# Optimization experiments

Hardware: AMD Instinct MI355X
Metric: run time of the kernel (lower is better)

## Reference

```python
import jax, jax.numpy as jnp
import numpy as np
import math

FACTOR = 100.0
WN_THRESH = 0.99

# extra MANO palm-closing faces from the original module
FACES_NEW = np.array([[92, 38, 234], [234, 38, 239], [38, 122, 239], [239, 122, 279],
                      [122, 118, 279], [279, 118, 215], [118, 117, 215], [215, 117, 214],
                      [117, 119, 214], [214, 119, 121], [119, 120, 121], [121, 120, 78],
                      [120, 108, 78], [78, 108, 79]], dtype=np.int64)


def solid_angles(points, triangles):
    # points: (B,Q,3); triangles: (B,F,3,3) -> (B,Q,F)
    ct = triangles[:, None] - points[:, :, None, None]        # (B,Q,F,3,3)
    norms = jnp.linalg.norm(ct, axis=-1)                      # (B,Q,F,3)
    cross = jnp.cross(ct[..., 1, :], ct[..., 2, :])           # (B,Q,F,3)
    numerator = jnp.sum(ct[..., 0, :] * cross, axis=-1)       # (B,Q,F)
    dot01 = jnp.sum(ct[..., 0, :] * ct[..., 1, :], axis=-1)
    dot12 = jnp.sum(ct[..., 1, :] * ct[..., 2, :], axis=-1)
    dot02 = jnp.sum(ct[..., 0, :] * ct[..., 2, :], axis=-1)
    denominator = (norms.prod(axis=-1) + dot01 * norms[..., 2]
                   + dot02 * norms[..., 1] + dot12 * norms[..., 0])
    return 2.0 * jnp.arctan2(numerator, denominator)


def winding_numbers(points, triangles):
    return solid_angles(points, triangles).sum(axis=-1) / (4.0 * math.pi)


def pairwise_dist(x, y, squared=False):
    # x: (B,N,3), y: (B,M,3) -> (B,N,M)
    xx = jnp.sum(x * x, axis=-1)
    yy = jnp.sum(y * y, axis=-1)
    zz = jnp.einsum('bnd,bmd->bnm', x, y)
    P = xx[:, :, None] + yy[:, None, :] - 2.0 * zz
    if not squared:
        P = jnp.sqrt(jnp.clip(P, 0.0))
    return P


def setup_inputs() -> dict:
    key = jax.random.key(0)
    k1, k2, k3 = jax.random.split(key, 3)
    B, Q, NF = 8, 778, 1538
    v1 = jax.random.normal(k1, (B, Q, 3), dtype=jnp.float32)
    v2 = jax.random.normal(k2, (B, Q, 3), dtype=jnp.float32)
    faces = jax.random.randint(k3, (NF, 3), 0, Q, dtype=jnp.int64)
    return {"v1": v1, "v2": v2, "faces": faces}


def reference(v1, v2, faces):
    r_faces = jnp.concatenate([faces, jnp.asarray(FACES_NEW)], axis=0)   # (F,3)
    l_faces = r_faces[:, jnp.array([0, 2, 1])]
    t1l = v1[:, l_faces, :]   # (B,F,3,3)
    t2l = v2[:, r_faces, :]
    interior_v1 = winding_numbers(v1, t2l) >= WN_THRESH   # (B,Q) bool
    interior_v2 = winding_numbers(v2, t1l) >= WN_THRESH

    d12 = pairwise_dist(v1, v2)       # (B,Q,Q)
    d21 = pairwise_dist(v2, v1)
    min12 = jnp.min(d12, axis=-1)     # (B,Q): dist from each v1 point to v2
    min21 = jnp.min(d21, axis=-1)

    pt1 = ((min12 * FACTOR) ** 2) * interior_v1.astype(v1.dtype)
    pt2 = ((min21 * FACTOR) ** 2) * interior_v2.astype(v2.dtype)
    bloss = pt1.sum(axis=-1) + pt2.sum(axis=-1)   # (B,)
    gate = jnp.any(interior_v1, axis=-1) & jnp.any(interior_v2, axis=-1)
    bloss = jnp.where(gate, bloss, 0.0)
    return bloss.mean()
```

## Files before the change

### kernel.cpp

```cpp
#include <hip/hip_runtime.h>
#include <math.h>

#define BQ 778
#define NF_IN 1538
#define NF_NEW 14
#define NT 1552
#define NB 8
#define BLOCK 1024
#define NWAVE 16
#define TRI_PER_WAVE 97

__constant__ int FACES_NEW_D[NF_NEW * 3] = {
    92, 38, 234, 234, 38, 239, 38, 122, 239, 239, 122, 279,
    122, 118, 279, 279, 118, 215, 118, 117, 215, 215, 117, 214,
    117, 119, 214, 214, 119, 121, 119, 120, 121, 121, 120, 78,
    120, 108, 78, 78, 108, 79};

__device__ __forceinline__ float fast_atan2f(float y, float x) {
  float ax = __builtin_fabsf(x), ay = __builtin_fabsf(y);
  float mx = fmaxf(ax, ay), mn = fminf(ax, ay);
  float r  = __builtin_amdgcn_rcpf(mx);
  float t  = mn * r;
  float e  = __builtin_fmaf(-t, mx, mn);
  t = __builtin_fmaf(e, r, t);
  float s = t * t;
  float u =                  0.00282363896258175373077393f;
  u = __builtin_fmaf(u, s, -0.0159569028764963150024414f);
  u = __builtin_fmaf(u, s,  0.0425049886107444763183594f);
  u = __builtin_fmaf(u, s, -0.0748900920152664184570312f);
  u = __builtin_fmaf(u, s,  0.106347933411598205566406f);
  u = __builtin_fmaf(u, s, -0.142027363181114196777344f);
  u = __builtin_fmaf(u, s,  0.199926957488059997558594f);
  u = __builtin_fmaf(u, s, -0.333331018686294555664062f);
  float a = __builtin_fmaf(u * s, t, t);
  a = (ay > ax) ? (1.57079632679489662f - a) : a;
  a = (x < 0.0f) ? (3.14159265358979323f - a) : a;
  return __builtin_copysignf(a, y);
}

__global__ __launch_bounds__(BLOCK) void wn_dist_kernel(
    const float* __restrict__ v1, const float* __restrict__ v2,
    const int* __restrict__ faces, float* __restrict__ sums,
    unsigned int* __restrict__ flags) {
  __shared__ float4 sv[BQ];
  __shared__ ushort4 sf4[NT];
  __shared__ float romega[NWAVE][64];
  __shared__ float rdmin[NWAVE][64];

  const int PG = 13;
  int bid = blockIdx.x;
  int cloud = bid / PG;
  int pg = bid % PG;
  int side = cloud >> 3;
  int b = cloud & 7;

  const float* pts = (side == 0) ? (v1 + b * BQ * 3) : (v2 + b * BQ * 3);
  const float* opp = (side == 0) ? (v2 + b * BQ * 3) : (v1 + b * BQ * 3);

  int tid = threadIdx.x;
  for (int i = tid; i < BQ; i += BLOCK) {
    sv[i] = make_float4(opp[i * 3 + 0], opp[i * 3 + 1], opp[i * 3 + 2], 0.0f);
  }
  for (int f = tid; f < NF_IN; f += BLOCK) {
    ushort4 u;
    u.x = (unsigned short)(faces[f * 3 + 0] << 4);
    u.y = (unsigned short)(faces[f * 3 + 1] << 4);
    u.z = (unsigned short)(faces[f * 3 + 2] << 4);
    u.w = 0;
    sf4[f] = u;
  }
  for (int f = tid; f < NF_NEW; f += BLOCK) {
    ushort4 u;
    u.x = (unsigned short)(FACES_NEW_D[f * 3 + 0] << 4);
    u.y = (unsigned short)(FACES_NEW_D[f * 3 + 1] << 4);
    u.z = (unsigned short)(FACES_NEW_D[f * 3 + 2] << 4);
    u.w = 0;
    sf4[NF_IN + f] = u;
  }
  __syncthreads();

  int wave = tid >> 6;
  int lane = tid & 63;
  int q = pg * 64 + lane;
  bool valid = (q < BQ);
  int qc = valid ? q : (BQ - 1);

  const float sgn = side ? -1.0f : 1.0f;
  float px = pts[qc * 3 + 0];
  float py = pts[qc * 3 + 1];
  float pz = pts[qc * 3 + 2];

  const char* svb = (const char*)sv;

  float omega = 0.0f;
  int tbase = wave * TRI_PER_WAVE;
  for (int k = 0; k < TRI_PER_WAVE; ++k) {
    ushort4 f = sf4[tbase + k];
    float4 va = *(const float4*)(svb + f.x);
    float4 vb = *(const float4*)(svb + f.y);
    float4 vc = *(const float4*)(svb + f.z);
    float ax = va.x - px, ay = va.y - py, az = va.z - pz;
    float bx = vb.x - px, by = vb.y - py, bz = vb.z - pz;
    float cx = vc.x - px, cy = vc.y - py, cz = vc.z - pz;
    float la = sqrtf(ax * ax + ay * ay + az * az);
    float lb = sqrtf(bx * bx + by * by + bz * bz);
    float lc = sqrtf(cx * cx + cy * cy + cz * cz);
    float crx = by * cz - bz * cy;
    float cry = bz * cx - bx * cz;
    float crz = bx * cy - by * cx;
    float num = ax * crx + ay * cry + az * crz;
    float d01 = ax * bx + ay * by + az * bz;
    float d02 = ax * cx + ay * cy + az * cz;
    float d12 = bx * cx + by * cy + bz * cz;
    float den = la * lb * lc + d01 * lc + d02 * lb + d12 * la;
    omega += fast_atan2f(sgn * num, den);
  }

  float dmin = 3.402823466e38f;
  for (int j = wave; j < BQ; j += NWAVE) {
    float4 vj = sv[j];
    float dx = vj.x - px, dy = vj.y - py, dz = vj.z - pz;
    dmin = fminf(dmin, dx * dx + dy * dy + dz * dz);
  }

  romega[wave][lane] = omega;
  rdmin[wave][lane] = dmin;
  __syncthreads();

  if (wave == 0) {
    float om = 0.0f;
    float dm = 3.402823466e38f;
#pragma unroll
    for (int w = 0; w < NWAVE; ++w) {
      om += romega[w][lane];
      dm = fminf(dm, rdmin[w][lane]);
    }
    float wn = om * 0.15915494309189535f;
    bool interior = valid && (wn >= 0.99f);
    float pt = interior ? fmaxf(dm, 0.0f) * 10000.0f : 0.0f;
    for (int off = 32; off; off >>= 1) pt += __shfl_xor(pt, off);
    bool anyint = __any(interior);
    if (lane == 0) {
      atomicAdd(&sums[cloud], pt);
      if (anyint) atomicOr(&flags[cloud], 1u);
    }
  }
}

__global__ void finalize_kernel(const float* __restrict__ sums,
                                const unsigned int* __restrict__ flags,
                                float* __restrict__ out) {
  if (threadIdx.x == 0) {
    float total = 0.0f;
    for (int b = 0; b < NB; ++b) {
      bool gate = (flags[b] != 0u) && (flags[NB + b] != 0u);
      if (gate) total += sums[b] + sums[NB + b];
    }
    out[0] = total * (1.0f / NB);
  }
}

extern "C" void kernel_launch(void* const* d_in, const int* in_sizes, int n_in,
                              void* d_out, int out_size, void* d_ws,
                              size_t ws_size, hipStream_t stream) {
  const float* v1 = (const float*)d_in[0];
  const float* v2 = (const float*)d_in[1];
  const int* faces = (const int*)d_in[2];
  float* out = (float*)d_out;

  float* sums = (float*)d_ws;
  unsigned int* flags = (unsigned int*)(sums + 16);

  hipMemsetAsync(d_ws, 0, 16 * sizeof(float) + 16 * sizeof(unsigned int),
                 stream);

  int grid = 16 * 13;
  wn_dist_kernel<<<grid, BLOCK, 0, stream>>>(v1, v2, faces, sums, flags);
  finalize_kernel<<<1, 64, 0, stream>>>(sums, flags, out);
}
```

Before: 150.2 us.

## Split triangle loop across 4x more blocks with partial buffers and separate reduce kernel

Each query group is now processed by four 512-thread blocks, each taking a quarter of the triangles and of the distance candidates, instead of one 1024-thread block. This gives 832 blocks rather than 208, so more CUs are filled. Per-point partial winding sums and minimum distances go to workspace, and a new reduce kernel combines them, replacing the atomics and the memset. The hardware sqrt intrinsic and loop unrolling are also used. In exchange, every block reloads the shared vertex and face tables and there is an extra kernel launch.

```diff
diff --git a/kernel.cpp b/kernel.cpp
--- a/kernel.cpp
+++ b/kernel.cpp
@@ -6,9 +6,11 @@
 #define NF_NEW 14
 #define NT 1552
 #define NB 8
-#define BLOCK 1024
-#define NWAVE 16
-#define TRI_PER_WAVE 97
+#define BLOCK 512
+#define NWAVE 8
+#define NSPLIT 4
+#define NSLOT 32
+#define PG 13
 
 __constant__ int FACES_NEW_D[NF_NEW * 3] = {
     92, 38, 234, 234, 38, 239, 38, 122, 239, 239, 122, 279,
@@ -38,19 +40,20 @@
   return __builtin_copysignf(a, y);
 }
 
-__global__ __launch_bounds__(BLOCK) void wn_dist_kernel(
+__global__ __launch_bounds__(BLOCK) void wn_part_kernel(
     const float* __restrict__ v1, const float* __restrict__ v2,
-    const int* __restrict__ faces, float* __restrict__ sums,
-    unsigned int* __restrict__ flags) {
+    const int* __restrict__ faces,
+    float* __restrict__ omega_part, float* __restrict__ dmin_part) {
   __shared__ float4 sv[BQ];
   __shared__ ushort4 sf4[NT];
   __shared__ float romega[NWAVE][64];
   __shared__ float rdmin[NWAVE][64];
 
-  const int PG = 13;
   int bid = blockIdx.x;
-  int cloud = bid / PG;
-  int pg = bid % PG;
+  int split = bid & (NSPLIT - 1);
+  int rest = bid >> 2;
+  int pg = rest % PG;
+  int cloud = rest / PG;
   int side = cloud >> 3;
   int b = cloud & 7;
 
@@ -92,19 +95,23 @@
 
   const char* svb = (const char*)sv;
 
+  int slot = split * NWAVE + wave;
+  int tstart = slot * 48 + (slot < 16 ? slot : 16);
+  int tcount = (slot < 16) ? 49 : 48;
+
   float omega = 0.0f;
-  int tbase = wave * TRI_PER_WAVE;
-  for (int k = 0; k < TRI_PER_WAVE; ++k) {
-    ushort4 f = sf4[tbase + k];
+#pragma unroll 2
+  for (int k = 0; k < tcount; ++k) {
+    ushort4 f = sf4[tstart + k];
     float4 va = *(const float4*)(svb + f.x);
     float4 vb = *(const float4*)(svb + f.y);
     float4 vc = *(const float4*)(svb + f.z);
     float ax = va.x - px, ay = va.y - py, az = va.z - pz;
     float bx = vb.x - px, by = vb.y - py, bz = vb.z - pz;
     float cx = vc.x - px, cy = vc.y - py, cz = vc.z - pz;
-    float la = sqrtf(ax * ax + ay * ay + az * az);
-    float lb = sqrtf(bx * bx + by * by + bz * bz);
-    float lc = sqrtf(cx * cx + cy * cy + cz * cz);
+    float la = __builtin_amdgcn_sqrtf(ax * ax + ay * ay + az * az);
+    float lb = __builtin_amdgcn_sqrtf(bx * bx + by * by + bz * bz);
+    float lc = __builtin_amdgcn_sqrtf(cx * cx + cy * cy + cz * cz);
     float crx = by * cz - bz * cy;
     float cry = bz * cx - bx * cz;
     float crz = bx * cy - by * cx;
@@ -117,7 +124,8 @@
   }
 
   float dmin = 3.402823466e38f;
-  for (int j = wave; j < BQ; j += NWAVE) {
+#pragma unroll 2
+  for (int j = slot; j < BQ; j += NSLOT) {
     float4 vj = sv[j];
     float dx = vj.x - px, dy = vj.y - py, dz = vj.z - pz;
     dmin = fminf(dmin, dx * dx + dy * dy + dz * dz);
@@ -127,7 +135,7 @@
   rdmin[wave][lane] = dmin;
   __syncthreads();
 
-  if (wave == 0) {
+  if (wave == 0 && valid) {
     float om = 0.0f;
     float dm = 3.402823466e38f;
 #pragma unroll
@@ -135,15 +143,45 @@
       om += romega[w][lane];
       dm = fminf(dm, rdmin[w][lane]);
     }
-    float wn = om * 0.15915494309189535f;
-    bool interior = valid && (wn >= 0.99f);
-    float pt = interior ? fmaxf(dm, 0.0f) * 10000.0f : 0.0f;
-    for (int off = 32; off; off >>= 1) pt += __shfl_xor(pt, off);
-    bool anyint = __any(interior);
-    if (lane == 0) {
-      atomicAdd(&sums[cloud], pt);
-      if (anyint) atomicOr(&flags[cloud], 1u);
-    }
+    int idx = (split * 16 + cloud) * BQ + q;
+    omega_part[idx] = om;
+    dmin_part[idx] = dm;
+  }
+}
+
+__global__ __launch_bounds__(1024) void reduce_kernel(
+    const float* __restrict__ omega_part, const float* __restrict__ dmin_part,
+    float* __restrict__ sums, unsigned int* __restrict__ flags) {
+  __shared__ float rs[1024];
+  __shared__ int ri[1024];
+  int cloud = blockIdx.x;
+  int p = threadIdx.x;
+
+  float om = 0.0f;
+  float dm = 3.402823466e38f;
+  if (p < BQ) {
+#pragma unroll
+    for (int s = 0; s < NSPLIT; ++s) {
+      int idx = (s * 16 + cloud) * BQ + p;
+      om += omega_part[idx];
+      dm = fminf(dm, dmin_part[idx]);
+    }
+  }
+  float wn = om * 0.15915494309189535f;
+  bool interior = (p < BQ) && (wn >= 0.99f);
+  rs[p] = interior ? fmaxf(dm, 0.0f) * 10000.0f : 0.0f;
+  ri[p] = interior ? 1 : 0;
+  __syncthreads();
+  for (int off = 512; off; off >>= 1) {
+    if (p < off) {
+      rs[p] += rs[p + off];
+      ri[p] |= ri[p + off];
+    }
+    __syncthreads();
+  }
+  if (p == 0) {
+    sums[cloud] = rs[0];
+    flags[cloud] = (unsigned int)ri[0];
   }
 }
 
@@ -168,13 +206,14 @@
   const int* faces = (const int*)d_in[2];
   float* out = (float*)d_out;
 
-  float* sums = (float*)d_ws;
+  float* omega_part = (float*)d_ws;
+  float* dmin_part = omega_part + NSPLIT * 16 * BQ;
+  float* sums = dmin_part + NSPLIT * 16 * BQ;
   unsigned int* flags = (unsigned int*)(sums + 16);
 
-  hipMemsetAsync(d_ws, 0, 16 * sizeof(float) + 16 * sizeof(unsigned int),
-                 stream);
-
-  int grid = 16 * 13;
-  wn_dist_kernel<<<grid, BLOCK, 0, stream>>>(v1, v2, faces, sums, flags);
+  int grid1 = 16 * PG * NSPLIT;
+  wn_part_kernel<<<grid1, BLOCK, 0, stream>>>(v1, v2, faces, omega_part,
+                                              dmin_part);
+  reduce_kernel<<<16, 1024, 0, stream>>>(omega_part, dmin_part, sums, flags);
   finalize_kernel<<<1, 64, 0, stream>>>(sums, flags, out);
 }
```

After: 122.6 us. 18.4% less time.
